# Kernel tuning notes

Measured on AMD Instinct MI355X. Metric: run time of the kernel, lower is better.

The kernel has to match this reference:

```python
import math
import jax, jax.numpy as jnp
import numpy as np

D_MODEL = 256
NUM_HEAD = 8
NUM_LEVEL = 1
KERNEL = 5
NUM_POINT = KERNEL * KERNEL
NUM_VAR = 5  # with_rotation=True
HEAD_DIM = D_MODEL // NUM_HEAD


def _kernel_indices(k=KERNEL):
    # odd kernel: linspace(-(k-1)/2, (k-1)/2, k); torch.meshgrid default 'ij'; stack([j,i])/k
    idx = jnp.linspace(-(k - 1) / 2.0, (k - 1) / 2.0, k)
    ii, jj = jnp.meshgrid(idx, idx, indexing='ij')
    return jnp.stack([jj, ii], axis=-1).reshape(-1, 2) / k  # (P, 2)


def setup_inputs() -> dict:
    key = jax.random.key(0)
    ks = jax.random.split(key, 8)
    B, LQ = 2, 4096
    Hf, Wf = 188, 188
    LV = Hf * Wf
    d = D_MODEL
    nb = NUM_LEVEL * NUM_HEAD * NUM_VAR
    na = NUM_HEAD * NUM_LEVEL * NUM_POINT
    return {
        'query': jax.random.normal(ks[0], (B, LQ, d), jnp.float32),
        'value': jax.random.normal(ks[1], (B, LV, d), jnp.float32),
        'ref_windows': jax.random.uniform(ks[2], (B, LQ, 7), jnp.float32),
        'W_box': jax.random.normal(ks[3], (nb, d), jnp.float32) * 0.02,
        'b_box': jax.random.uniform(ks[4], (nb,), jnp.float32),
        'W_attn': jax.random.normal(ks[5], (na, d), jnp.float32) * 0.02,
        'b_attn': jnp.zeros((na,), jnp.float32),
        'W_value': jax.random.normal(ks[6], (d, d), jnp.float32) * 0.02,
        'b_value': jnp.zeros((d,), jnp.float32),
        'W_out': jax.random.normal(ks[7], (d, d), jnp.float32) * 0.02,
        'b_out': jnp.zeros((d,), jnp.float32),
        'H_feat': Hf,
        'W_feat': Wf,
    }


def reference(query, value, ref_windows, W_box, b_box, W_attn, b_attn,
              W_value, b_value, W_out, b_out, H_feat, W_feat):
    B, LQ, d = query.shape
    LV = value.shape[1]
    Hh, Lv, P, Dh = NUM_HEAD, NUM_LEVEL, NUM_POINT, HEAD_DIM

    # value projection -> (B, LV, Hh, Dh)
    v = (value @ W_value.T + b_value).reshape(B, LV, Hh, Dh)

    # attention weights: softmax over (level*point) per head
    attn = jax.nn.softmax((query @ W_attn.T + b_attn).reshape(B, LQ, Hh, Lv * P), axis=-1)
    attn = attn.reshape(B, LQ, Hh, Lv, P)

    # --- _where_to_attend ---
    ob = (query @ W_box.T + b_box).reshape(B, LQ, Hh, Lv, NUM_VAR)
    rw = ref_windows[:, :, None, None, :]                    # (B,LQ,1,1,7)
    ref_boxes = rw[..., jnp.array([0, 1, 3, 4])]             # cx, cy, w, h
    ref_angles = rw[..., 6:7]
    off_boxes, off_angles = ob[..., :4], ob[..., 4:5]
    angles = (ref_angles + off_angles / 16.0) * (2.0 * math.pi)
    boxes = ref_boxes + off_boxes / 8.0 * ref_boxes[..., jnp.array([2, 3, 2, 3])]
    center = boxes[..., None, :2]                            # (B,LQ,Hh,Lv,1,2)
    size = boxes[..., None, 2:4]
    cos_a, sin_a = jnp.cos(angles), jnp.sin(angles)
    rot = jnp.stack([cos_a, -sin_a, sin_a, cos_a], axis=-1).reshape(B, LQ, Hh, Lv, 1, 2, 2)
    g = _kernel_indices() * jax.nn.relu(size)                # (B,LQ,Hh,Lv,P,2)
    grid = center + (g[..., None, :] * rot).sum(-1)          # (B,LQ,Hh,Lv,P,2), normalized [0,1]

    # --- single-level bilinear sampling (align_corners=False, zero padding) ---
    gl = grid[:, :, :, 0]                                    # (B,LQ,Hh,P,2)
    gx = gl[..., 0] * W_feat - 0.5
    gy = gl[..., 1] * H_feat - 0.5
    x0 = jnp.floor(gx)
    y0 = jnp.floor(gy)
    x0i = x0.astype(jnp.int32)
    y0i = y0.astype(jnp.int32)
    wx1 = gx - x0
    wy1 = gy - y0
    wx0 = 1.0 - wx1
    wy0 = 1.0 - wy1

    b_idx = jnp.arange(B)[:, None, None, None]
    h_idx = jnp.arange(Hh)[None, None, :, None]

    def gather(yi, xi):
        valid = (xi >= 0) & (xi < W_feat) & (yi >= 0) & (yi < H_feat)
        lin = jnp.clip(yi, 0, H_feat - 1) * W_feat + jnp.clip(xi, 0, W_feat - 1)
        return v[b_idx, lin, h_idx] * valid[..., None]       # (B,LQ,Hh,P,Dh)

    s = (gather(y0i, x0i) * (wy0 * wx0)[..., None]
         + gather(y0i, x0i + 1) * (wy0 * wx1)[..., None]
         + gather(y0i + 1, x0i) * (wy1 * wx0)[..., None]
         + gather(y0i + 1, x0i + 1) * (wy1 * wx1)[..., None])

    out_heads = (s * attn[:, :, :, 0, :, None]).sum(axis=3)  # (B,LQ,Hh,Dh)
    out = out_heads.reshape(B, LQ, Hh * Dh) @ W_out.T + b_out
    attn_w = attn.reshape(B, LQ, Hh, Lv, KERNEL, KERNEL)
    return out, attn_w
```

## Files before the change

### kernel.cpp

```cpp
#include <hip/hip_runtime.h>


typedef float floatx4 __attribute__((ext_vector_type(4)));
typedef short shortx8 __attribute__((ext_vector_type(8)));

static __device__ __forceinline__ unsigned short f2bf(float x) {
    unsigned int u = __float_as_uint(x);
    return (unsigned short)((u + 0x7fffu + ((u >> 16) & 1u)) >> 16);
}
static __device__ __forceinline__ unsigned int pack2(float a, float b) {
    return (unsigned int)f2bf(a) | ((unsigned int)f2bf(b) << 16);
}
static __device__ __forceinline__ void async16(const void* g, void* lds) {
    __builtin_amdgcn_global_load_lds(
        (const __attribute__((address_space(1))) unsigned int*)g,
        (__attribute__((address_space(3))) unsigned int*)lds, 16, 0, 0);
}

__global__ __launch_bounds__(256) void convert_kernel(
    const float* __restrict__ value, unsigned short* __restrict__ vbf, long long nv4,
    const float* __restrict__ W_value, unsigned short* __restrict__ wvbf,
    const float* __restrict__ W_attn, const float* __restrict__ W_box,
    unsigned short* __restrict__ wabf, float* __restrict__ Wab,
    const float* __restrict__ W_out, unsigned short* __restrict__ wobf,
    const float* __restrict__ b_attn, const float* __restrict__ b_box,
    float* __restrict__ bab)
{
    const int NBV = 2048;
    const int blk = blockIdx.x, tid = threadIdx.x;
    if (blk < NBV) {
        for (long long i = (long long)blk * 256 + tid; i < nv4; i += (long long)NBV * 256) {
            float4 f = ((const float4*)value)[i];
            ((uint2*)vbf)[i] = make_uint2(pack2(f.x, f.y), pack2(f.z, f.w));
        }
    } else if (blk < NBV + 16) {
        int base = (blk - NBV) * 1024 + tid;
#pragma unroll
        for (int k = 0; k < 4; ++k) {
            int j = base + k * 256;
            float4 f = ((const float4*)W_value)[j];
            ((uint2*)wvbf)[j] = make_uint2(pack2(f.x, f.y), pack2(f.z, f.w));
        }
    } else if (blk < NBV + 32) {
        int base = (blk - NBV - 16) * 1024 + tid;
#pragma unroll
        for (int k = 0; k < 4; ++k) {
            int j = base + k * 256;
            int row = j >> 6, col = (j & 63) * 4;
            float4 f;
            if (row < 200)      f = *(const float4*)(W_attn + (size_t)row * 256 + col);
            else if (row < 240) f = *(const float4*)(W_box + (size_t)(row - 200) * 256 + col);
            else                f = make_float4(0.f, 0.f, 0.f, 0.f);
            ((uint2*)wabf)[j] = make_uint2(pack2(f.x, f.y), pack2(f.z, f.w));
            ((float4*)Wab)[j] = f;
        }
    } else if (blk < NBV + 48) {
        int base = (blk - NBV - 32) * 1024 + tid;
#pragma unroll
        for (int k = 0; k < 4; ++k) {
            int j = base + k * 256;
            float4 f = ((const float4*)W_out)[j];
            ((uint2*)wobf)[j] = make_uint2(pack2(f.x, f.y), pack2(f.z, f.w));
        }
    } else {
        bab[tid] = tid < 200 ? b_attn[tid] : (tid < 240 ? b_box[tid - 200] : 0.f);
    }
}

__global__ __launch_bounds__(256) void convert_oh(
    const float* __restrict__ src, unsigned short* __restrict__ dst)
{
    int base = blockIdx.x * 256 + threadIdx.x;
#pragma unroll
    for (int k = 0; k < 8; ++k) {
        int j = base + k * 65536;
        float4 f = ((const float4*)src)[j];
        ((uint2*)dst)[j] = make_uint2(pack2(f.x, f.y), pack2(f.z, f.w));
    }
}

template <int OUTMODE>
__global__ __launch_bounds__(256) void gemm_bf16(
    const unsigned short* __restrict__ A,
    const unsigned short* __restrict__ Bw,
    const float* __restrict__ bias,
    void* __restrict__ Cv, int M, int LV)
{
    __shared__ unsigned short As[128 * 64];
    __shared__ unsigned short Bs[128 * 64];
    const int tid = threadIdx.x;
    const int wv = tid >> 6, lane = tid & 63;
    const int lr = lane & 15, lq = lane >> 4;
    const int m0 = blockIdx.x * 128, n0 = blockIdx.y * 128;
    const int wm = wv & 1, wn = wv >> 1;
    const int srow = tid >> 3;
    const int scol = (tid & 7) * 8;

    floatx4 acc[4][4];
#pragma unroll
    for (int i = 0; i < 4; ++i)
#pragma unroll
        for (int j = 0; j < 4; ++j) acc[i][j] = (floatx4){0.f, 0.f, 0.f, 0.f};

    for (int kc = 0; kc < 4; ++kc) {
        const int k0 = kc * 64;
        __syncthreads();
#pragma unroll
        for (int i = 0; i < 4; ++i) {
            int ra = m0 + i * 32 + srow; ra = ra < M ? ra : M - 1;
            async16(A + (size_t)ra * 256 + k0 + scol, (char*)As + i * 4096 + wv * 1024);
            int rb = n0 + i * 32 + srow;
            async16(Bw + (size_t)rb * 256 + k0 + scol, (char*)Bs + i * 4096 + wv * 1024);
        }
        __syncthreads();
#pragma unroll
        for (int kk = 0; kk < 64; kk += 32) {
            shortx8 af[4], bfr[4];
#pragma unroll
            for (int t = 0; t < 4; ++t) {
                af[t]  = *(const shortx8*)&As[(wm * 64 + t * 16 + lr) * 64 + kk + lq * 8];
                bfr[t] = *(const shortx8*)&Bs[(wn * 64 + t * 16 + lr) * 64 + kk + lq * 8];
            }
#pragma unroll
            for (int ti = 0; ti < 4; ++ti)
#pragma unroll
                for (int tj = 0; tj < 4; ++tj)
                    acc[ti][tj] = __builtin_amdgcn_mfma_f32_16x16x32_bf16(af[ti], bfr[tj], acc[ti][tj], 0, 0, 0);
        }
    }
#pragma unroll
    for (int tj = 0; tj < 4; ++tj) {
        int n = n0 + wn * 64 + tj * 16 + lr;
        float bv = bias[n];
#pragma unroll
        for (int ti = 0; ti < 4; ++ti) {
#pragma unroll
            for (int r = 0; r < 4; ++r) {
                int m = m0 + wm * 64 + ti * 16 + lq * 4 + r;
                if (m >= M) continue;
                float val = acc[ti][tj][r] + bv;
                if (OUTMODE == 0) {
                    ((float*)Cv)[(size_t)m * 256 + n] = val;
                } else {
                    int h = n >> 5, dh = n & 31;
                    int b = m >= LV ? 1 : 0;
                    int lv = m - (b ? LV : 0);
                    ((unsigned short*)Cv)[((size_t)(b * 8 + h) * LV + lv) * 32 + dh] = f2bf(val);
                }
            }
        }
    }
}

__global__ __launch_bounds__(256) void gemm_nt_bias(
    const float* __restrict__ A, const float* __restrict__ W,
    const float* __restrict__ bias, float* __restrict__ C, int M)
{
    const int K = 256, N = 256;
    __shared__ float As[16][68];
    __shared__ float Bs[16][68];
    int tid = threadIdx.x;
    int tcol = tid & 15, trow = tid >> 4;
    int m0 = blockIdx.x * 64, n0 = blockIdx.y * 64;
    int lr = tid >> 2, lc = (tid & 3) << 2;
    float acc[4][4] = {};
    for (int k0 = 0; k0 < K; k0 += 16) {
        int arow = m0 + lr; if (arow > M - 1) arow = M - 1;
        float4 av = *(const float4*)(A + (size_t)arow * K + k0 + lc);
        float4 wv = *(const float4*)(W + (size_t)(n0 + lr) * K + k0 + lc);
        __syncthreads();
        As[lc + 0][lr] = av.x; As[lc + 1][lr] = av.y; As[lc + 2][lr] = av.z; As[lc + 3][lr] = av.w;
        Bs[lc + 0][lr] = wv.x; Bs[lc + 1][lr] = wv.y; Bs[lc + 2][lr] = wv.z; Bs[lc + 3][lr] = wv.w;
        __syncthreads();
#pragma unroll
        for (int k = 0; k < 16; ++k) {
            float4 a4 = *(const float4*)&As[k][trow << 2];
            float4 b4 = *(const float4*)&Bs[k][tcol << 2];
            float a[4] = {a4.x, a4.y, a4.z, a4.w};
            float bb[4] = {b4.x, b4.y, b4.z, b4.w};
#pragma unroll
            for (int i = 0; i < 4; i++)
#pragma unroll
                for (int j = 0; j < 4; j++) acc[i][j] += a[i] * bb[j];
        }
    }
#pragma unroll
    for (int i = 0; i < 4; i++) {
        int m = m0 + trow * 4 + i;
        if (m >= M) continue;
#pragma unroll
        for (int j = 0; j < 4; j++) {
            int n = n0 + tcol * 4 + j;
            C[(size_t)m * N + n] = acc[i][j] + bias[n];
        }
    }
}

__global__ __launch_bounds__(256) void decode_sample_kernel(
    const unsigned short* __restrict__ v,
    const float* __restrict__ logits,
    const float* __restrict__ ref_windows,
    float* __restrict__ attn_out,
    float* __restrict__ out_heads,
    const int* __restrict__ Hf_p, const int* __restrict__ Wf_p, int LV, int LQ)
{
    __shared__ float lg[8][32];
    __shared__ float rw[8][7];
    __shared__ float prm[8][6];
    __shared__ float mxinv[8][2];
    __shared__ float4 wls[8][25];
    __shared__ int2 bls[8][25];

    const int s = blockIdx.x, c = blockIdx.y;
    const int b = s >> 3, h = s & 7;
    const int tid = threadIdx.x;
    const int Hf = *Hf_p, Wf = *Wf_p;
    const size_t mbase = (size_t)b * LQ + c * 8;

    if (tid < 240) {
        int qq = tid / 30, j = tid - qq * 30;
        int col = (j < 25) ? h * 25 + j : 200 + h * 5 + (j - 25);
        lg[qq][j] = logits[(mbase + qq) * 256 + col];
    }
    if (tid < 56) {
        int qq = tid / 7, k = tid - qq * 7;
        rw[qq][k] = ref_windows[(mbase + qq) * 7 + k];
    }
    __syncthreads();

    if (tid < 8) {
        int qq = tid;
        float mx = -1e30f;
#pragma unroll
        for (int p = 0; p < 25; p++) mx = fmaxf(mx, lg[qq][p]);
        float ssum = 0.f;
#pragma unroll
        for (int p = 0; p < 25; p++) ssum += expf(lg[qq][p] - mx);
        mxinv[qq][0] = mx; mxinv[qq][1] = 1.f / ssum;
        float cx = rw[qq][0] + lg[qq][25] * 0.125f * rw[qq][3];
        float cy = rw[qq][1] + lg[qq][26] * 0.125f * rw[qq][4];
        float bw = rw[qq][3] + lg[qq][27] * 0.125f * rw[qq][3];
        float bh = rw[qq][4] + lg[qq][28] * 0.125f * rw[qq][4];
        float ang = (rw[qq][6] + lg[qq][29] * 0.0625f) * 6.283185307179586f;
        prm[qq][0] = cx; prm[qq][1] = cy;
        prm[qq][2] = fmaxf(bw, 0.f); prm[qq][3] = fmaxf(bh, 0.f);
        prm[qq][4] = cosf(ang); prm[qq][5] = sinf(ang);
    }
    __syncthreads();

    if (tid < 200) {
        int qq = tid / 25, p = tid - qq * 25;
        float a = expf(lg[qq][p] - mxinv[qq][0]) * mxinv[qq][1];
        attn_out[(mbase + qq) * 200 + h * 25 + p] = a;
        int pi = p / 5, pj = p - pi * 5;
        float g0 = (float)(pj - 2) * 0.2f * prm[qq][2];
        float g1 = (float)(pi - 2) * 0.2f * prm[qq][3];
        float ca = prm[qq][4], sa = prm[qq][5];
        float gx = (prm[qq][0] + g0 * ca - g1 * sa) * (float)Wf - 0.5f;
        float gy = (prm[qq][1] + g0 * sa + g1 * ca) * (float)Hf - 0.5f;
        float x0f = floorf(gx), y0f = floorf(gy);
        int x0 = (int)x0f, y0 = (int)y0f;
        float wx1 = gx - x0f, wy1 = gy - y0f;
        float wx0 = 1.f - wx1, wy0 = 1.f - wy1;
        int y1 = y0 + 1;
        int bx; float wl, wr;
        if (x0 >= 0 && x0 <= Wf - 2)      { bx = x0;     wl = wx0; wr = wx1; }
        else if (x0 == -1)                { bx = 0;      wl = wx1; wr = 0.f; }
        else if (x0 == Wf - 1)            { bx = Wf - 2; wl = 0.f; wr = wx0; }
        else                              { bx = 0;      wl = 0.f; wr = 0.f; }
        float wy0v = (y0 >= 0 && y0 < Hf) ? wy0 : 0.f;
        float wy1v = (y1 >= 0 && y1 < Hf) ? wy1 : 0.f;
        int cy0 = min(max(y0, 0), Hf - 1), cy1 = min(max(y1, 0), Hf - 1);
        float4 wv4;
        wv4.x = a * wy0v * wl; wv4.y = a * wy0v * wr;
        wv4.z = a * wy1v * wl; wv4.w = a * wy1v * wr;
        wls[qq][p] = wv4;
        bls[qq][p] = make_int2(cy0 * Wf + bx, cy1 * Wf + bx);
    }
    __syncthreads();

    const int qq = tid >> 5, l = tid & 31;
    const unsigned int* vw = (const unsigned int*)(v + (size_t)s * LV * 32);
    const int colsel = l >> 4;
    float a0 = 0.f, a1 = 0.f;
#pragma unroll
    for (int p = 0; p < 25; ++p) {
        float4 w = wls[qq][p];
        int2 rb = bls[qq][p];
        unsigned int u0 = vw[(size_t)rb.x * 16 + l];
        unsigned int u1 = vw[(size_t)rb.y * 16 + l];
        float w0 = colsel ? w.y : w.x;
        float w1 = colsel ? w.w : w.z;
        a0 += w0 * __uint_as_float(u0 << 16) + w1 * __uint_as_float(u1 << 16);
        a1 += w0 * __uint_as_float(u0 & 0xffff0000u) + w1 * __uint_as_float(u1 & 0xffff0000u);
    }
    a0 += __shfl_xor(a0, 16, 32);
    a1 += __shfl_xor(a1, 16, 32);
    if (l < 16)
        *(float2*)(out_heads + (mbase + qq) * 256 + h * 32 + 2 * l) = make_float2(a0, a1);
}

extern "C" void kernel_launch(void* const* d_in, const int* in_sizes, int n_in,
                              void* d_out, int out_size, void* d_ws, size_t ws_size,
                              hipStream_t stream) {
    const float* query       = (const float*)d_in[0];
    const float* value       = (const float*)d_in[1];
    const float* ref_windows = (const float*)d_in[2];
    const float* W_box       = (const float*)d_in[3];
    const float* b_box       = (const float*)d_in[4];
    const float* W_attn      = (const float*)d_in[5];
    const float* b_attn      = (const float*)d_in[6];
    const float* W_value     = (const float*)d_in[7];
    const float* b_value     = (const float*)d_in[8];
    const float* W_out       = (const float*)d_in[9];
    const float* b_out       = (const float*)d_in[10];
    const int*   Hf          = (const int*)d_in[11];
    const int*   Wf          = (const int*)d_in[12];

    const int M1 = in_sizes[1] / 256;
    const int MQ = in_sizes[0] / 256;
    const int LQ = MQ / 2;
    const int LV = M1 / 2;

    unsigned short* vbf  = (unsigned short*)d_ws;
    unsigned short* Vout = vbf + (size_t)M1 * 256;
    unsigned short* ohbf = Vout + (size_t)M1 * 256;
    unsigned short* wvbf = ohbf + (size_t)MQ * 256;
    unsigned short* wabf = wvbf + 65536;
    unsigned short* wobf = wabf + 65536;
    float* Wab       = (float*)(wobf + 65536);
    float* bab       = Wab + 65536;
    float* logits    = bab + 256;
    float* out_heads = logits + (size_t)MQ * 256;

    float* out0     = (float*)d_out;
    float* attn_out = out0 + (size_t)MQ * 256;

    const long long nv4 = (long long)M1 * 64;

    convert_kernel<<<2097, 256, 0, stream>>>(value, vbf, nv4, W_value, wvbf,
                                             W_attn, W_box, wabf, Wab,
                                             W_out, wobf, b_attn, b_box, bab);
    dim3 g1((M1 + 127) / 128, 2);
    gemm_bf16<1><<<g1, 256, 0, stream>>>(vbf, wvbf, b_value, Vout, M1, LV);
    dim3 g2(MQ / 64, 4);
    gemm_nt_bias<<<g2, 256, 0, stream>>>(query, Wab, bab, logits, MQ);
    decode_sample_kernel<<<dim3(16, LQ / 8), 256, 0, stream>>>(
        Vout, logits, ref_windows, attn_out, out_heads, Hf, Wf, LV, LQ);
    convert_oh<<<256, 256, 0, stream>>>(out_heads, ohbf);
    dim3 g4(MQ / 128, 2);
    gemm_bf16<0><<<g4, 256, 0, stream>>>(ohbf, wobf, b_out, out0, MQ, LV);
}
```

Measured before the change: 249.2 us.

## Fuse bf16 conversion into sampler and vectorize GEMM epilogue stores

The sampling kernel now writes its per-head outputs directly as packed bf16, which removes the separate convert_oh launch and its fp32 round trip through memory. The GEMM swaps MFMA operand order so each lane holds four consecutive output columns, letting the epilogue issue float4 or packed-bf16 uint2 stores instead of scalar ones. The sampler also precomputes pre-scaled offsets and per-column-half weights in a packed LDS table and splits the accumulators to shorten dependency chains. It relies on bias and row offsets being 16-byte aligned.

Measured after the change: 222.2 us. 10.8% less time.

```diff
diff --git a/kernel.cpp b/kernel.cpp
--- a/kernel.cpp
+++ b/kernel.cpp
@@ -64,18 +64,6 @@
         }
     } else {
         bab[tid] = tid < 200 ? b_attn[tid] : (tid < 240 ? b_box[tid - 200] : 0.f);
-    }
-}
-
-__global__ __launch_bounds__(256) void convert_oh(
-    const float* __restrict__ src, unsigned short* __restrict__ dst)
-{
-    int base = blockIdx.x * 256 + threadIdx.x;
-#pragma unroll
-    for (int k = 0; k < 8; ++k) {
-        int j = base + k * 65536;
-        float4 f = ((const float4*)src)[j];
-        ((uint2*)dst)[j] = make_uint2(pack2(f.x, f.y), pack2(f.z, f.w));
     }
 }
 
@@ -125,28 +113,34 @@
             for (int ti = 0; ti < 4; ++ti)
 #pragma unroll
                 for (int tj = 0; tj < 4; ++tj)
-                    acc[ti][tj] = __builtin_amdgcn_mfma_f32_16x16x32_bf16(af[ti], bfr[tj], acc[ti][tj], 0, 0, 0);
-        }
-    }
-#pragma unroll
-    for (int tj = 0; tj < 4; ++tj) {
-        int n = n0 + wn * 64 + tj * 16 + lr;
-        float bv = bias[n];
-#pragma unroll
-        for (int ti = 0; ti < 4; ++ti) {
-#pragma unroll
-            for (int r = 0; r < 4; ++r) {
-                int m = m0 + wm * 64 + ti * 16 + lq * 4 + r;
-                if (m >= M) continue;
-                float val = acc[ti][tj][r] + bv;
-                if (OUTMODE == 0) {
-                    ((float*)Cv)[(size_t)m * 256 + n] = val;
-                } else {
-                    int h = n >> 5, dh = n & 31;
-                    int b = m >= LV ? 1 : 0;
-                    int lv = m - (b ? LV : 0);
-                    ((unsigned short*)Cv)[((size_t)(b * 8 + h) * LV + lv) * 32 + dh] = f2bf(val);
-                }
+                    acc[ti][tj] = __builtin_amdgcn_mfma_f32_16x16x32_bf16(bfr[tj], af[ti], acc[ti][tj], 0, 0, 0);
+        }
+    }
+#pragma unroll
+    for (int ti = 0; ti < 4; ++ti) {
+        int m = m0 + wm * 64 + ti * 16 + lr;
+        if (m >= M) continue;
+        if (OUTMODE == 0) {
+            float* Crow = (float*)Cv + (size_t)m * 256;
+#pragma unroll
+            for (int tj = 0; tj < 4; ++tj) {
+                int nb = n0 + wn * 64 + tj * 16 + lq * 4;
+                float4 bv = *(const float4*)(bias + nb);
+                float4 o = make_float4(acc[ti][tj][0] + bv.x, acc[ti][tj][1] + bv.y,
+                                       acc[ti][tj][2] + bv.z, acc[ti][tj][3] + bv.w);
+                *(float4*)(Crow + nb) = o;
+            }
+        } else {
+            int b = m >= LV ? 1 : 0;
+            int lv = m - (b ? LV : 0);
+#pragma unroll
+            for (int tj = 0; tj < 4; ++tj) {
+                int nb = n0 + wn * 64 + tj * 16 + lq * 4;
+                float4 bv = *(const float4*)(bias + nb);
+                int h = nb >> 5, dh = nb & 31;
+                unsigned short* dst = (unsigned short*)Cv + ((size_t)(b * 8 + h) * LV + lv) * 32 + dh;
+                *(uint2*)dst = make_uint2(pack2(acc[ti][tj][0] + bv.x, acc[ti][tj][1] + bv.y),
+                                          pack2(acc[ti][tj][2] + bv.z, acc[ti][tj][3] + bv.w));
             }
         }
     }
@@ -201,15 +195,14 @@
     const float* __restrict__ logits,
     const float* __restrict__ ref_windows,
     float* __restrict__ attn_out,
-    float* __restrict__ out_heads,
+    unsigned short* __restrict__ ohbf,
     const int* __restrict__ Hf_p, const int* __restrict__ Wf_p, int LV, int LQ)
 {
     __shared__ float lg[8][32];
     __shared__ float rw[8][7];
     __shared__ float prm[8][6];
     __shared__ float mxinv[8][2];
-    __shared__ float4 wls[8][25];
-    __shared__ int2 bls[8][25];
+    __shared__ uint4 pk[8][25][2];
 
     const int s = blockIdx.x, c = blockIdx.y;
     const int b = s >> 3, h = s & 7;
@@ -271,33 +264,34 @@
         float wy0v = (y0 >= 0 && y0 < Hf) ? wy0 : 0.f;
         float wy1v = (y1 >= 0 && y1 < Hf) ? wy1 : 0.f;
         int cy0 = min(max(y0, 0), Hf - 1), cy1 = min(max(y1, 0), Hf - 1);
-        float4 wv4;
-        wv4.x = a * wy0v * wl; wv4.y = a * wy0v * wr;
-        wv4.z = a * wy1v * wl; wv4.w = a * wy1v * wr;
-        wls[qq][p] = wv4;
-        bls[qq][p] = make_int2(cy0 * Wf + bx, cy1 * Wf + bx);
+        unsigned off0 = (unsigned)(cy0 * Wf + bx) * 16u;
+        unsigned off1 = (unsigned)(cy1 * Wf + bx) * 16u;
+        float aw0 = a * wy0v, aw1 = a * wy1v;
+        pk[qq][p][0] = make_uint4(__float_as_uint(aw0 * wl), __float_as_uint(aw1 * wl), off0, off1);
+        pk[qq][p][1] = make_uint4(__float_as_uint(aw0 * wr), __float_as_uint(aw1 * wr), off0, off1);
     }
     __syncthreads();
 
     const int qq = tid >> 5, l = tid & 31;
     const unsigned int* vw = (const unsigned int*)(v + (size_t)s * LV * 32);
-    const int colsel = l >> 4;
-    float a0 = 0.f, a1 = 0.f;
+    const uint4* pkp = &pk[qq][0][l >> 4];
+    float e0 = 0.f, o0 = 0.f, e1 = 0.f, o1 = 0.f;
 #pragma unroll
     for (int p = 0; p < 25; ++p) {
-        float4 w = wls[qq][p];
-        int2 rb = bls[qq][p];
-        unsigned int u0 = vw[(size_t)rb.x * 16 + l];
-        unsigned int u1 = vw[(size_t)rb.y * 16 + l];
-        float w0 = colsel ? w.y : w.x;
-        float w1 = colsel ? w.w : w.z;
-        a0 += w0 * __uint_as_float(u0 << 16) + w1 * __uint_as_float(u1 << 16);
-        a1 += w0 * __uint_as_float(u0 & 0xffff0000u) + w1 * __uint_as_float(u1 & 0xffff0000u);
-    }
+        uint4 t = pkp[2 * p];
+        float w0 = __uint_as_float(t.x), w1 = __uint_as_float(t.y);
+        unsigned u0 = vw[t.z + l];
+        unsigned u1 = vw[t.w + l];
+        e0 += w0 * __uint_as_float(u0 << 16);
+        o0 += w0 * __uint_as_float(u0 & 0xffff0000u);
+        e1 += w1 * __uint_as_float(u1 << 16);
+        o1 += w1 * __uint_as_float(u1 & 0xffff0000u);
+    }
+    float a0 = e0 + e1, a1 = o0 + o1;
     a0 += __shfl_xor(a0, 16, 32);
     a1 += __shfl_xor(a1, 16, 32);
     if (l < 16)
-        *(float2*)(out_heads + (mbase + qq) * 256 + h * 32 + 2 * l) = make_float2(a0, a1);
+        ((unsigned int*)ohbf)[(mbase + qq) * 128 + h * 16 + l] = pack2(a0, a1);
 }
 
 extern "C" void kernel_launch(void* const* d_in, const int* in_sizes, int n_in,
@@ -331,7 +325,6 @@
     float* Wab       = (float*)(wobf + 65536);
     float* bab       = Wab + 65536;
     float* logits    = bab + 256;
-    float* out_heads = logits + (size_t)MQ * 256;
 
     float* out0     = (float*)d_out;
     float* attn_out = out0 + (size_t)MQ * 256;
@@ -346,8 +339,7 @@
     dim3 g2(MQ / 64, 4);
     gemm_nt_bias<<<g2, 256, 0, stream>>>(query, Wab, bab, logits, MQ);
     decode_sample_kernel<<<dim3(16, LQ / 8), 256, 0, stream>>>(
-        Vout, logits, ref_windows, attn_out, out_heads, Hf, Wf, LV, LQ);
-    convert_oh<<<256, 256, 0, stream>>>(out_heads, ohbf);
+        Vout, logits, ref_windows, attn_out, ohbf, Hf, Wf, LV, LQ);
     dim3 g4(MQ / 128, 2);
     gemm_bf16<0><<<g4, 256, 0, stream>>>(ohbf, wobf, b_out, out0, MQ, LV);
 }
```
